# Kernel optimization log

Measured on AMD Instinct MI355X. Metric: run time of the kernel, lower is better.

## Reference

```python
import jax, jax.numpy as jnp
import numpy as np

N = 50000      # nodes
E = 400000     # edges (avg degree 8)
N_IN = 256     # n_in_chan
N_HID = 256    # n_hid_chan


def gcn_conv(x, src, dst, W, b, n):
    """PyG GCNConv: D^{-1/2}(A+I)D^{-1/2} X W^T + b (add_self_loops=True, unit weights)."""
    h = x @ W.T                                           # [n, out]
    # degree over A + I: each node has a self loop (the initial ones) plus in-edges
    deg = jnp.ones((n,), h.dtype).at[dst].add(1.0)        # [n]
    dinv = jax.lax.rsqrt(deg)                             # deg >= 1 always
    norm = dinv[src] * dinv[dst]                          # [E]
    agg = jnp.zeros_like(h).at[dst].add(h[src] * norm[:, None])
    agg = agg + h * (dinv * dinv)[:, None]                # self-loop term, norm = dinv_i^2
    return agg + b


def setup_inputs() -> dict:
    key = jax.random.key(0)
    k1, k2, k3, k4 = jax.random.split(key, 4)
    x = jax.random.normal(k1, (N, N_IN + N_HID), dtype=jnp.float32)
    edge_index = jax.random.randint(k2, (2, E), 0, N, dtype=jnp.int64)
    s1 = 1.0 / np.sqrt(N_IN + N_HID)
    s2 = 1.0 / np.sqrt(N_HID)
    W1 = jax.random.normal(k3, (N_HID, N_IN + N_HID), dtype=jnp.float32) * s1
    W2 = jax.random.normal(k4, (N_HID, N_HID), dtype=jnp.float32) * s2
    b1 = jnp.zeros((N_HID,), jnp.float32)
    b2 = jnp.zeros((N_HID,), jnp.float32)
    return {"x": x, "edge_index": edge_index, "W1": W1, "b1": b1, "W2": W2, "b2": b2}


def reference(x, edge_index, W1, b1, W2, b2):
    src, dst = edge_index[0], edge_index[1]
    h = jax.nn.relu(gcn_conv(x, src, dst, W1, b1, N))
    return gcn_conv(h, src, dst, W2, b2, N)
```

## Files before the change

kernel.cpp:

```cpp
#include <hip/hip_runtime.h>
#include <hip/hip_bf16.h>

#define NN 50000
#define CH 256
#define SLOTS 96
#define G1K 512
#define G2K 256

typedef unsigned short u16;
typedef unsigned int   u32;

using short8 = __attribute__((ext_vector_type(8))) short;
using u16x8  = __attribute__((ext_vector_type(8))) unsigned short;
using f32x4  = __attribute__((ext_vector_type(4))) float;

static __device__ __forceinline__ float4 ld4(const float* p){ return *(const float4*)p; }

static __device__ __forceinline__ u16 f2b(float f){
  u32 u = __float_as_uint(f);
  u = (u + 0x7fffu + ((u >> 16) & 1u)) >> 16;
  return (u16)u;
}
static __device__ __forceinline__ float b2f(u16 b){
  return __uint_as_float(((u32)b) << 16);
}
static __device__ __forceinline__ int pkbf(float lo, float hi){
  __hip_bfloat162 h = __float22bfloat162_rn(make_float2(lo, hi));
  int r; __builtin_memcpy(&r, &h, 4); return r;
}

static __device__ __forceinline__ void gload_lds16(const u16* g, u16* l){
  __builtin_amdgcn_global_load_lds((const __attribute__((address_space(1))) void*)g,
                                   (__attribute__((address_space(3))) void*)l, 16, 0, 0);
}

#define WBAR(vm) do{ \
    asm volatile("s_waitcnt vmcnt(" #vm ") lgkmcnt(0)" ::: "memory"); \
    __builtin_amdgcn_s_barrier(); \
  }while(0)


__global__ void ell_build_kernel(const int* __restrict__ src, const int* __restrict__ dst,
                                 int* __restrict__ deg, int* __restrict__ ell, int E,
                                 const float* __restrict__ W1, u16* __restrict__ W1bf, int w1n4,
                                 const float* __restrict__ W2, u16* __restrict__ W2bf, int w2n4){
  int T = gridDim.x * 256;
  int g = blockIdx.x*256 + threadIdx.x;
  if (g < E){
    int d = dst[g];
    int pos = atomicAdd(&deg[d], 1);
    if (pos < SLOTS) ell[(size_t)d*SLOTS + pos] = src[g];
  }
  for (int i = g; i < w1n4; i += T){
    float4 v = ld4(W1 + (size_t)i*4);
    ushort4 o; o.x=f2b(v.x); o.y=f2b(v.y); o.z=f2b(v.z); o.w=f2b(v.w);
    *(ushort4*)(W1bf + (size_t)i*4) = o;
  }
  for (int i = g; i < w2n4; i += T){
    float4 v = ld4(W2 + (size_t)i*4);
    ushort4 o; o.x=f2b(v.x); o.y=f2b(v.y); o.z=f2b(v.z); o.w=f2b(v.w);
    *(ushort4*)(W2bf + (size_t)i*4) = o;
  }
}


#define G1_GLB(kt, bb) do{ \
    gload_lds16(gB + (size_t)(kt)*32,               &Bs[bb][wave*2048]); \
    gload_lds16(gB + (size_t)(kt)*32 + 16*G1K,      &Bs[bb][wave*2048 + 512]); \
    gload_lds16(gB + (size_t)(kt)*32 + 32*G1K,      &Bs[bb][wave*2048 + 1024]); \
    gload_lds16(gB + (size_t)(kt)*32 + 48*G1K,      &Bs[bb][wave*2048 + 1536]); \
  }while(0)

#define G1_LA(S, k0) do{ \
    A##S##a = ld4(ga + (k0)); A##S##b = ld4(ga + (k0) + 4); \
  }while(0)

#define G1_SA(S) do{ \
    int4 _w = { pkbf(A##S##a.x,A##S##a.y), pkbf(A##S##a.z,A##S##a.w), \
                pkbf(A##S##b.x,A##S##b.y), pkbf(A##S##b.z,A##S##b.w) }; \
    *(int4*)&As[S][aoff] = _w; \
  }while(0)

#define G1_COMP(ra, rb) do{ \
    short8 af[4], bq[4]; \
    _Pragma("unroll") \
    for (int i=0;i<4;i++) af[i] = *(const short8*)&As[ra][(i*16 + lm)*32 + lk]; \
    _Pragma("unroll") \
    for (int j=0;j<4;j++) bq[j] = *(const short8*)&Bs[rb][(wave*64 + j*16 + lm)*32 + lk]; \
    _Pragma("unroll") \
    for (int i=0;i<4;i++) \
      _Pragma("unroll") \
      for (int j=0;j<4;j++) \
        acc[i][j] = __builtin_amdgcn_mfma_f32_16x16x32_bf16(af[i], bq[j], acc[i][j], 0, 0, 0); \
  }while(0)

__global__ __launch_bounds__(256, 4) void gemm1_kernel(const float* __restrict__ A,
                                                       const u16* __restrict__ Bbf,
                                                       u16* __restrict__ C, int M){
  __shared__ u16 As[2][64*32];
  __shared__ u16 Bs[2][256*32];
  int tid = threadIdx.x;
  int wave = tid >> 6, lane = tid & 63;
  int bm = blockIdx.x;

  int sra = tid >> 2;
  int sca = (tid & 3) * 8;
  int ar = bm*64 + sra; if (ar > M-1) ar = M-1;
  const float* ga = A + (size_t)ar*G1K + sca;
  int aoff = sra*32 + sca;
  const u16* gB = Bbf + (size_t)(wave*64 + (lane>>2))*G1K + (lane&3)*8;

  int lm = lane & 15;
  int lk = (lane >> 4) * 8;

  f32x4 acc[4][4] = {};

  float4 A0a,A0b;
  float4 A1a,A1b;

  G1_GLB(0, 0);
  G1_LA(0, 0);
  G1_LA(1, 32);
  G1_SA(0);
  G1_LA(0, 64);
  asm volatile("s_waitcnt vmcnt(0) lgkmcnt(0)" ::: "memory");
  __builtin_amdgcn_s_barrier();

  G1_GLB( 1,1); G1_COMP(0,0); G1_SA(1); G1_LA(1, 96); WBAR(2);
  G1_GLB( 2,0); G1_COMP(1,1); G1_SA(0); G1_LA(0,128); WBAR(2);
  G1_GLB( 3,1); G1_COMP(0,0); G1_SA(1); G1_LA(1,160); WBAR(2);
  G1_GLB( 4,0); G1_COMP(1,1); G1_SA(0); G1_LA(0,192); WBAR(2);
  G1_GLB( 5,1); G1_COMP(0,0); G1_SA(1); G1_LA(1,224); WBAR(2);
  G1_GLB( 6,0); G1_COMP(1,1); G1_SA(0); G1_LA(0,256); WBAR(2);
  G1_GLB( 7,1); G1_COMP(0,0); G1_SA(1); G1_LA(1,288); WBAR(2);
  G1_GLB( 8,0); G1_COMP(1,1); G1_SA(0); G1_LA(0,320); WBAR(2);
  G1_GLB( 9,1); G1_COMP(0,0); G1_SA(1); G1_LA(1,352); WBAR(2);
  G1_GLB(10,0); G1_COMP(1,1); G1_SA(0); G1_LA(0,384); WBAR(2);
  G1_GLB(11,1); G1_COMP(0,0); G1_SA(1); G1_LA(1,416); WBAR(2);
  G1_GLB(12,0); G1_COMP(1,1); G1_SA(0); G1_LA(0,448); WBAR(2);
  G1_GLB(13,1); G1_COMP(0,0); G1_SA(1); G1_LA(1,480); WBAR(2);
  G1_GLB(14,0); G1_COMP(1,1); G1_SA(0);               WBAR(0);
  G1_GLB(15,1); G1_COMP(0,0); G1_SA(1);               WBAR(0);
                G1_COMP(1,1);

  int rb = (lane >> 4) * 4;
  #pragma unroll
  for (int i=0;i<4;i++){
    #pragma unroll
    for (int r=0;r<4;r++){
      int row = bm*64 + i*16 + rb + r;
      if (row < M){
        #pragma unroll
        for (int j=0;j<4;j++){
          int col = wave*64 + j*16 + lm;
          C[(size_t)row*CH + col] = f2b(acc[i][j][r]);
        }
      }
    }
  }
}


#define G2_GLB(kt, bb) do{ \
    gload_lds16(gA + (size_t)(kt)*32,          &As2[bb][wave*512]); \
    gload_lds16(gB + (size_t)(kt)*32,          &Bs2[bb][wave*2048]); \
    gload_lds16(gB + (size_t)(kt)*32 + 16*G2K, &Bs2[bb][wave*2048 + 512]); \
    gload_lds16(gB + (size_t)(kt)*32 + 32*G2K, &Bs2[bb][wave*2048 + 1024]); \
    gload_lds16(gB + (size_t)(kt)*32 + 48*G2K, &Bs2[bb][wave*2048 + 1536]); \
  }while(0)

#define G2_COMP(rb) do{ \
    short8 af[4], bq[4]; \
    _Pragma("unroll") \
    for (int i=0;i<4;i++) af[i] = *(const short8*)&As2[rb][(i*16 + lm)*32 + lk]; \
    _Pragma("unroll") \
    for (int j=0;j<4;j++) bq[j] = *(const short8*)&Bs2[rb][(wave*64 + j*16 + lm)*32 + lk]; \
    _Pragma("unroll") \
    for (int i=0;i<4;i++) \
      _Pragma("unroll") \
      for (int j=0;j<4;j++) \
        acc[i][j] = __builtin_amdgcn_mfma_f32_16x16x32_bf16(af[i], bq[j], acc[i][j], 0, 0, 0); \
  }while(0)

__global__ __launch_bounds__(256, 4) void gemm2_kernel(const u16* __restrict__ A,
                                                       const u16* __restrict__ B,
                                                       u16* __restrict__ C, int M){
  __shared__ u16 As2[2][64*32];
  __shared__ u16 Bs2[2][256*32];
  int tid = threadIdx.x;
  int wave = tid >> 6, lane = tid & 63;
  int bm = blockIdx.x;

  int ar = bm*64 + wave*16 + (lane>>2); if (ar > M-1) ar = M-1;
  const u16* gA = A + (size_t)ar*G2K + (lane&3)*8;
  const u16* gB = B + (size_t)(wave*64 + (lane>>2))*G2K + (lane&3)*8;

  int lm = lane & 15;
  int lk = (lane >> 4) * 8;

  f32x4 acc[4][4] = {};

  G2_GLB(0, 0);
  asm volatile("s_waitcnt vmcnt(0)" ::: "memory");
  __builtin_amdgcn_s_barrier();

  G2_GLB(1, 1); G2_COMP(0); WBAR(0);
  G2_GLB(2, 0); G2_COMP(1); WBAR(0);
  G2_GLB(3, 1); G2_COMP(0); WBAR(0);
  G2_GLB(4, 0); G2_COMP(1); WBAR(0);
  G2_GLB(5, 1); G2_COMP(0); WBAR(0);
  G2_GLB(6, 0); G2_COMP(1); WBAR(0);
  G2_GLB(7, 1); G2_COMP(0); WBAR(0);
                G2_COMP(1);

  int rb = (lane >> 4) * 4;
  #pragma unroll
  for (int i=0;i<4;i++){
    #pragma unroll
    for (int r=0;r<4;r++){
      int row = bm*64 + i*16 + rb + r;
      if (row < M){
        #pragma unroll
        for (int j=0;j<4;j++){
          int col = wave*64 + j*16 + lm;
          C[(size_t)row*CH + col] = f2b(acc[i][j][r]);
        }
      }
    }
  }
}


template<bool RELU, bool OUTBF>
__global__ __launch_bounds__(256) void aggregate_kernel(const u16* __restrict__ h,
                                                        const float* __restrict__ bias,
                                                        const int* __restrict__ deg,
                                                        const int* __restrict__ ell,
                                                        void* __restrict__ outv, int n){
  int wave = threadIdx.x >> 6;
  int lane = threadIdx.x & 63;
  int i = blockIdx.x*4 + wave;
  if (i >= n) return;
  int half = lane >> 5;
  int c = (lane & 31) * 8;

  int degi = deg[i];
  float di = rsqrtf(1.0f + (float)degi);
  int m = degi < SLOTS ? degi : SLOTS;
  const int* row = ell + (size_t)i*SLOTS;

  float acc[8];
  #pragma unroll
  for (int k=0;k<8;k++) acc[k] = 0.f;

  int e = half;
  for (; e + 6 < m; e += 8){
    int s0 = row[e],   s1 = row[e+2], s2 = row[e+4], s3 = row[e+6];
    float n0 = rsqrtf(1.0f + (float)deg[s0]) * di;
    float n1 = rsqrtf(1.0f + (float)deg[s1]) * di;
    float n2 = rsqrtf(1.0f + (float)deg[s2]) * di;
    float n3 = rsqrtf(1.0f + (float)deg[s3]) * di;
    u16x8 h0 = *(const u16x8*)(h + (size_t)s0*CH + c);
    u16x8 h1 = *(const u16x8*)(h + (size_t)s1*CH + c);
    u16x8 h2 = *(const u16x8*)(h + (size_t)s2*CH + c);
    u16x8 h3 = *(const u16x8*)(h + (size_t)s3*CH + c);
    #pragma unroll
    for (int k=0;k<8;k++) acc[k] += b2f(h0[k])*n0;
    #pragma unroll
    for (int k=0;k<8;k++) acc[k] += b2f(h1[k])*n1;
    #pragma unroll
    for (int k=0;k<8;k++) acc[k] += b2f(h2[k])*n2;
    #pragma unroll
    for (int k=0;k<8;k++) acc[k] += b2f(h3[k])*n3;
  }
  for (; e < m; e += 2){
    int s0 = row[e];
    float n0 = rsqrtf(1.0f + (float)deg[s0]) * di;
    u16x8 h0 = *(const u16x8*)(h + (size_t)s0*CH + c);
    #pragma unroll
    for (int k=0;k<8;k++) acc[k] += b2f(h0[k])*n0;
  }

  if (half == 0){
    float w = di*di;
    float4 b0 = ld4(bias + c), b1 = ld4(bias + c + 4);
    u16x8 hv = *(const u16x8*)(h + (size_t)i*CH + c);
    acc[0] += b2f(hv[0])*w + b0.x; acc[1] += b2f(hv[1])*w + b0.y;
    acc[2] += b2f(hv[2])*w + b0.z; acc[3] += b2f(hv[3])*w + b0.w;
    acc[4] += b2f(hv[4])*w + b1.x; acc[5] += b2f(hv[5])*w + b1.y;
    acc[6] += b2f(hv[6])*w + b1.z; acc[7] += b2f(hv[7])*w + b1.w;
  }

  #pragma unroll
  for (int k=0;k<8;k++) acc[k] += __shfl_xor(acc[k], 32, 64);

  if (half == 0){
    if (RELU){
      #pragma unroll
      for (int k=0;k<8;k++) acc[k] = fmaxf(acc[k], 0.f);
    }
    if (OUTBF){
      u16x8 o;
      #pragma unroll
      for (int k=0;k<8;k++) o[k] = f2b(acc[k]);
      *(u16x8*)((u16*)outv + (size_t)i*CH + c) = o;
    } else {
      float* op = (float*)outv + (size_t)i*CH + c;
      *(float4*)op       = make_float4(acc[0],acc[1],acc[2],acc[3]);
      *(float4*)(op + 4) = make_float4(acc[4],acc[5],acc[6],acc[7]);
    }
  }
}


extern "C" void kernel_launch(void* const* d_in, const int* in_sizes, int n_in,
                              void* d_out, int out_size, void* d_ws, size_t ws_size,
                              hipStream_t stream){
  const float* x  = (const float*)d_in[0];
  const int*   ei = (const int*)d_in[1];
  const float* W1 = (const float*)d_in[2];
  const float* b1 = (const float*)d_in[3];
  const float* W2 = (const float*)d_in[4];
  const float* b2 = (const float*)d_in[5];
  float* out = (float*)d_out;

  const int n = NN;
  const int E = in_sizes[1] / 2;
  const int* src = ei;
  const int* dst = ei + E;

  char* ws = (char*)d_ws;
  size_t off = 0;
  auto alloc = [&](size_t bytes)->char* {
    char* p = ws + off;
    off += (bytes + 255) & ~(size_t)255;
    return p;
  };
  u16*   h1bf   = (u16*)  alloc((size_t)n*CH*sizeof(u16));
  u16*   g2out  = (u16*)  alloc((size_t)n*CH*sizeof(u16));
  u16*   W1bf   = (u16*)  alloc((size_t)CH*G1K*sizeof(u16));
  u16*   W2bf   = (u16*)  alloc((size_t)CH*CH*sizeof(u16));
  int*   deg    = (int*)  alloc((size_t)n*sizeof(int));
  int*   ell    = (int*)  alloc((size_t)n*SLOTS*sizeof(int));
  (void)ws_size;

  u16* g1out = (u16*)d_out;

  hipMemsetAsync(deg, 0, (size_t)n*sizeof(int), stream);
  ell_build_kernel<<<(E+255)/256, 256, 0, stream>>>(src, dst, deg, ell, E,
                                                    W1, W1bf, CH*G1K/4,
                                                    W2, W2bf, CH*CH/4);

  dim3 gg((n+63)/64);
  gemm1_kernel<<<gg, 256, 0, stream>>>(x, W1bf, g1out, n);
  aggregate_kernel<true, true><<<(n+3)/4, 256, 0, stream>>>(g1out, b1, deg, ell, h1bf, n);

  gemm2_kernel<<<gg, 256, 0, stream>>>(h1bf, W2bf, g2out, n);
  aggregate_kernel<false, false><<<(n+3)/4, 256, 0, stream>>>(g2out, b2, deg, ell, out, n);
}
```

Before: 316.9 us.

## Reorder layer-2 aggregate before GEMM, pre-convert X to bf16, triple-buffer GEMMs

Layer 2 now aggregates h1 first and multiplies by W2 afterwards (A(hW)=(Ah)W), with the bias moved into the GEMM epilogue and fp32 output written straight from the GEMM. X is converted to bf16 in the prep kernel so GEMM1 can load A with direct global-to-LDS loads. Both GEMMs move from double to triple buffering with a deeper vmcnt wait. The risk is the extra full pass over X (read fp32, write bf16) in the prep kernel, which may cost more than the simpler GEMM1 A-path saves.

```diff
diff --git a/kernel.cpp b/kernel.cpp
--- a/kernel.cpp
+++ b/kernel.cpp
@@ -42,6 +42,7 @@
 
 __global__ void ell_build_kernel(const int* __restrict__ src, const int* __restrict__ dst,
                                  int* __restrict__ deg, int* __restrict__ ell, int E,
+                                 const float* __restrict__ X,  u16* __restrict__ Xbf,  int xn4,
                                  const float* __restrict__ W1, u16* __restrict__ W1bf, int w1n4,
                                  const float* __restrict__ W2, u16* __restrict__ W2bf, int w2n4){
   int T = gridDim.x * 256;
@@ -51,40 +52,36 @@
     int pos = atomicAdd(&deg[d], 1);
     if (pos < SLOTS) ell[(size_t)d*SLOTS + pos] = src[g];
   }
+  for (int i = g; i < xn4; i += T){
+    float4 v = ld4(X + (size_t)i*4);
+    int2 o = { pkbf(v.x,v.y), pkbf(v.z,v.w) };
+    *(int2*)(Xbf + (size_t)i*4) = o;
+  }
   for (int i = g; i < w1n4; i += T){
     float4 v = ld4(W1 + (size_t)i*4);
-    ushort4 o; o.x=f2b(v.x); o.y=f2b(v.y); o.z=f2b(v.z); o.w=f2b(v.w);
-    *(ushort4*)(W1bf + (size_t)i*4) = o;
+    int2 o = { pkbf(v.x,v.y), pkbf(v.z,v.w) };
+    *(int2*)(W1bf + (size_t)i*4) = o;
   }
   for (int i = g; i < w2n4; i += T){
     float4 v = ld4(W2 + (size_t)i*4);
-    ushort4 o; o.x=f2b(v.x); o.y=f2b(v.y); o.z=f2b(v.z); o.w=f2b(v.w);
-    *(ushort4*)(W2bf + (size_t)i*4) = o;
+    int2 o = { pkbf(v.x,v.y), pkbf(v.z,v.w) };
+    *(int2*)(W2bf + (size_t)i*4) = o;
   }
 }
 
 
 #define G1_GLB(kt, bb) do{ \
-    gload_lds16(gB + (size_t)(kt)*32,               &Bs[bb][wave*2048]); \
-    gload_lds16(gB + (size_t)(kt)*32 + 16*G1K,      &Bs[bb][wave*2048 + 512]); \
-    gload_lds16(gB + (size_t)(kt)*32 + 32*G1K,      &Bs[bb][wave*2048 + 1024]); \
-    gload_lds16(gB + (size_t)(kt)*32 + 48*G1K,      &Bs[bb][wave*2048 + 1536]); \
-  }while(0)
-
-#define G1_LA(S, k0) do{ \
-    A##S##a = ld4(ga + (k0)); A##S##b = ld4(ga + (k0) + 4); \
-  }while(0)
-
-#define G1_SA(S) do{ \
-    int4 _w = { pkbf(A##S##a.x,A##S##a.y), pkbf(A##S##a.z,A##S##a.w), \
-                pkbf(A##S##b.x,A##S##b.y), pkbf(A##S##b.z,A##S##b.w) }; \
-    *(int4*)&As[S][aoff] = _w; \
-  }while(0)
-
-#define G1_COMP(ra, rb) do{ \
+    gload_lds16(gA + (size_t)(kt)*32,          &As[bb][wave*512]); \
+    gload_lds16(gB + (size_t)(kt)*32,          &Bs[bb][wave*2048]); \
+    gload_lds16(gB + (size_t)(kt)*32 + 16*G1K, &Bs[bb][wave*2048 + 512]); \
+    gload_lds16(gB + (size_t)(kt)*32 + 32*G1K, &Bs[bb][wave*2048 + 1024]); \
+    gload_lds16(gB + (size_t)(kt)*32 + 48*G1K, &Bs[bb][wave*2048 + 1536]); \
+  }while(0)
+
+#define G1_COMP(rb) do{ \
     short8 af[4], bq[4]; \
     _Pragma("unroll") \
-    for (int i=0;i<4;i++) af[i] = *(const short8*)&As[ra][(i*16 + lm)*32 + lk]; \
+    for (int i=0;i<4;i++) af[i] = *(const short8*)&As[rb][(i*16 + lm)*32 + lk]; \
     _Pragma("unroll") \
     for (int j=0;j<4;j++) bq[j] = *(const short8*)&Bs[rb][(wave*64 + j*16 + lm)*32 + lk]; \
     _Pragma("unroll") \
@@ -94,20 +91,17 @@
         acc[i][j] = __builtin_amdgcn_mfma_f32_16x16x32_bf16(af[i], bq[j], acc[i][j], 0, 0, 0); \
   }while(0)
 
-__global__ __launch_bounds__(256, 4) void gemm1_kernel(const float* __restrict__ A,
+__global__ __launch_bounds__(256, 4) void gemm1_kernel(const u16* __restrict__ A,
                                                        const u16* __restrict__ Bbf,
                                                        u16* __restrict__ C, int M){
-  __shared__ u16 As[2][64*32];
-  __shared__ u16 Bs[2][256*32];
+  __shared__ u16 As[3][64*32];
+  __shared__ u16 Bs[3][256*32];
   int tid = threadIdx.x;
   int wave = tid >> 6, lane = tid & 63;
   int bm = blockIdx.x;
 
-  int sra = tid >> 2;
-  int sca = (tid & 3) * 8;
-  int ar = bm*64 + sra; if (ar > M-1) ar = M-1;
-  const float* ga = A + (size_t)ar*G1K + sca;
-  int aoff = sra*32 + sca;
+  int ar = bm*64 + wave*16 + (lane>>2); if (ar > M-1) ar = M-1;
+  const u16* gA = A + (size_t)ar*G1K + (lane&3)*8;
   const u16* gB = Bbf + (size_t)(wave*64 + (lane>>2))*G1K + (lane&3)*8;
 
   int lm = lane & 15;
@@ -115,33 +109,26 @@
 
   f32x4 acc[4][4] = {};
 
-  float4 A0a,A0b;
-  float4 A1a,A1b;
-
   G1_GLB(0, 0);
-  G1_LA(0, 0);
-  G1_LA(1, 32);
-  G1_SA(0);
-  G1_LA(0, 64);
-  asm volatile("s_waitcnt vmcnt(0) lgkmcnt(0)" ::: "memory");
-  __builtin_amdgcn_s_barrier();
-
-  G1_GLB( 1,1); G1_COMP(0,0); G1_SA(1); G1_LA(1, 96); WBAR(2);
-  G1_GLB( 2,0); G1_COMP(1,1); G1_SA(0); G1_LA(0,128); WBAR(2);
-  G1_GLB( 3,1); G1_COMP(0,0); G1_SA(1); G1_LA(1,160); WBAR(2);
-  G1_GLB( 4,0); G1_COMP(1,1); G1_SA(0); G1_LA(0,192); WBAR(2);
-  G1_GLB( 5,1); G1_COMP(0,0); G1_SA(1); G1_LA(1,224); WBAR(2);
-  G1_GLB( 6,0); G1_COMP(1,1); G1_SA(0); G1_LA(0,256); WBAR(2);
-  G1_GLB( 7,1); G1_COMP(0,0); G1_SA(1); G1_LA(1,288); WBAR(2);
-  G1_GLB( 8,0); G1_COMP(1,1); G1_SA(0); G1_LA(0,320); WBAR(2);
-  G1_GLB( 9,1); G1_COMP(0,0); G1_SA(1); G1_LA(1,352); WBAR(2);
-  G1_GLB(10,0); G1_COMP(1,1); G1_SA(0); G1_LA(0,384); WBAR(2);
-  G1_GLB(11,1); G1_COMP(0,0); G1_SA(1); G1_LA(1,416); WBAR(2);
-  G1_GLB(12,0); G1_COMP(1,1); G1_SA(0); G1_LA(0,448); WBAR(2);
-  G1_GLB(13,1); G1_COMP(0,0); G1_SA(1); G1_LA(1,480); WBAR(2);
-  G1_GLB(14,0); G1_COMP(1,1); G1_SA(0);               WBAR(0);
-  G1_GLB(15,1); G1_COMP(0,0); G1_SA(1);               WBAR(0);
-                G1_COMP(1,1);
+  G1_GLB(1, 1);
+  WBAR(5);
+
+  G1_GLB( 2,2); G1_COMP(0); WBAR(5);
+  G1_GLB( 3,0); G1_COMP(1); WBAR(5);
+  G1_GLB( 4,1); G1_COMP(2); WBAR(5);
+  G1_GLB( 5,2); G1_COMP(0); WBAR(5);
+  G1_GLB( 6,0); G1_COMP(1); WBAR(5);
+  G1_GLB( 7,1); G1_COMP(2); WBAR(5);
+  G1_GLB( 8,2); G1_COMP(0); WBAR(5);
+  G1_GLB( 9,0); G1_COMP(1); WBAR(5);
+  G1_GLB(10,1); G1_COMP(2); WBAR(5);
+  G1_GLB(11,2); G1_COMP(0); WBAR(5);
+  G1_GLB(12,0); G1_COMP(1); WBAR(5);
+  G1_GLB(13,1); G1_COMP(2); WBAR(5);
+  G1_GLB(14,2); G1_COMP(0); WBAR(5);
+  G1_GLB(15,0); G1_COMP(1); WBAR(5);
+                G1_COMP(2); WBAR(0);
+                G1_COMP(0);
 
   int rb = (lane >> 4) * 4;
   #pragma unroll
@@ -184,9 +171,10 @@
 
 __global__ __launch_bounds__(256, 4) void gemm2_kernel(const u16* __restrict__ A,
                                                        const u16* __restrict__ B,
-                                                       u16* __restrict__ C, int M){
-  __shared__ u16 As2[2][64*32];
-  __shared__ u16 Bs2[2][256*32];
+                                                       float* __restrict__ Cout,
+                                                       const float* __restrict__ bias, int M){
+  __shared__ u16 As2[3][64*32];
+  __shared__ u16 Bs2[3][256*32];
   int tid = threadIdx.x;
   int wave = tid >> 6, lane = tid & 63;
   int bm = blockIdx.x;
@@ -201,17 +189,21 @@
   f32x4 acc[4][4] = {};
 
   G2_GLB(0, 0);
-  asm volatile("s_waitcnt vmcnt(0)" ::: "memory");
-  __builtin_amdgcn_s_barrier();
-
-  G2_GLB(1, 1); G2_COMP(0); WBAR(0);
-  G2_GLB(2, 0); G2_COMP(1); WBAR(0);
-  G2_GLB(3, 1); G2_COMP(0); WBAR(0);
-  G2_GLB(4, 0); G2_COMP(1); WBAR(0);
-  G2_GLB(5, 1); G2_COMP(0); WBAR(0);
-  G2_GLB(6, 0); G2_COMP(1); WBAR(0);
-  G2_GLB(7, 1); G2_COMP(0); WBAR(0);
-                G2_COMP(1);
+  G2_GLB(1, 1);
+  WBAR(5);
+
+  G2_GLB(2,2); G2_COMP(0); WBAR(5);
+  G2_GLB(3,0); G2_COMP(1); WBAR(5);
+  G2_GLB(4,1); G2_COMP(2); WBAR(5);
+  G2_GLB(5,2); G2_COMP(0); WBAR(5);
+  G2_GLB(6,0); G2_COMP(1); WBAR(5);
+  G2_GLB(7,1); G2_COMP(2); WBAR(5);
+               G2_COMP(0); WBAR(0);
+               G2_COMP(1);
+
+  float bv[4];
+  #pragma unroll
+  for (int j=0;j<4;j++) bv[j] = bias[wave*64 + j*16 + lm];
 
   int rb = (lane >> 4) * 4;
   #pragma unroll
@@ -223,7 +215,7 @@
         #pragma unroll
         for (int j=0;j<4;j++){
           int col = wave*64 + j*16 + lm;
-          C[(size_t)row*CH + col] = f2b(acc[i][j][r]);
+          Cout[(size_t)row*CH + col] = acc[i][j][r] + bv[j];
         }
       }
     }
@@ -231,7 +223,7 @@
 }
 
 
-template<bool RELU, bool OUTBF>
+template<bool RELU, bool BIAS, bool OUTBF>
 __global__ __launch_bounds__(256) void aggregate_kernel(const u16* __restrict__ h,
                                                         const float* __restrict__ bias,
                                                         const int* __restrict__ deg,
@@ -283,12 +275,14 @@
 
   if (half == 0){
     float w = di*di;
-    float4 b0 = ld4(bias + c), b1 = ld4(bias + c + 4);
     u16x8 hv = *(const u16x8*)(h + (size_t)i*CH + c);
-    acc[0] += b2f(hv[0])*w + b0.x; acc[1] += b2f(hv[1])*w + b0.y;
-    acc[2] += b2f(hv[2])*w + b0.z; acc[3] += b2f(hv[3])*w + b0.w;
-    acc[4] += b2f(hv[4])*w + b1.x; acc[5] += b2f(hv[5])*w + b1.y;
-    acc[6] += b2f(hv[6])*w + b1.z; acc[7] += b2f(hv[7])*w + b1.w;
+    #pragma unroll
+    for (int k=0;k<8;k++) acc[k] += b2f(hv[k])*w;
+    if (BIAS){
+      float4 b0 = ld4(bias + c), b1 = ld4(bias + c + 4);
+      acc[0] += b0.x; acc[1] += b0.y; acc[2] += b0.z; acc[3] += b0.w;
+      acc[4] += b1.x; acc[5] += b1.y; acc[6] += b1.z; acc[7] += b1.w;
+    }
   }
 
   #pragma unroll
@@ -336,8 +330,9 @@
     off += (bytes + 255) & ~(size_t)255;
     return p;
   };
+  u16*   xbf    = (u16*)  alloc((size_t)n*G1K*sizeof(u16));
   u16*   h1bf   = (u16*)  alloc((size_t)n*CH*sizeof(u16));
-  u16*   g2out  = (u16*)  alloc((size_t)n*CH*sizeof(u16));
+  u16*   h2bf   = (u16*)  alloc((size_t)n*CH*sizeof(u16));
   u16*   W1bf   = (u16*)  alloc((size_t)CH*G1K*sizeof(u16));
   u16*   W2bf   = (u16*)  alloc((size_t)CH*CH*sizeof(u16));
   int*   deg    = (int*)  alloc((size_t)n*sizeof(int));
@@ -348,13 +343,15 @@
 
   hipMemsetAsync(deg, 0, (size_t)n*sizeof(int), stream);
   ell_build_kernel<<<(E+255)/256, 256, 0, stream>>>(src, dst, deg, ell, E,
+                                                    x,  xbf,  n*G1K/4,
                                                     W1, W1bf, CH*G1K/4,
                                                     W2, W2bf, CH*CH/4);
 
   dim3 gg((n+63)/64);
-  gemm1_kernel<<<gg, 256, 0, stream>>>(x, W1bf, g1out, n);
-  aggregate_kernel<true, true><<<(n+3)/4, 256, 0, stream>>>(g1out, b1, deg, ell, h1bf, n);
-
-  gemm2_kernel<<<gg, 256, 0, stream>>>(h1bf, W2bf, g2out, n);
-  aggregate_kernel<false, false><<<(n+3)/4, 256, 0, stream>>>(g2out, b2, deg, ell, out, n);
-}
+
+  gemm1_kernel<<<gg, 256, 0, stream>>>(xbf, W1bf, g1out, n);
+  aggregate_kernel<true, true, true><<<(n+3)/4, 256, 0, stream>>>(g1out, b1, deg, ell, h1bf, n);
+
+  aggregate_kernel<false, false, true><<<(n+3)/4, 256, 0, stream>>>(h1bf, b2, deg, ell, h2bf, n);
+  gemm2_kernel<<<gg, 256, 0, stream>>>(h2bf, W2bf, out, b2, n);
+}
```

Result: slower. 333.6 us (+5.3%).
